# Optimization experiments

Measured on AMD Instinct MI355X. Metric: run time of the kernel, lower is better.

## Reference

```python
import jax, jax.numpy as jnp
import numpy as np

B = 8
N_KV = 1024          # kv-scale tokens (32x32)
D0, D1, D2 = 256, 512, 1024
DIM_HEAD = 64
H0, H2 = 2, 8        # fine-scale heads, coarse-scale heads (H2 == 4*H0)
EPS = 1e-5


def _ln(x, g, b):
    mu = jnp.mean(x, axis=-1, keepdims=True)
    var = jnp.var(x, axis=-1, keepdims=True)
    return (x - mu) * jax.lax.rsqrt(var + EPS) * g + b


def setup_inputs() -> dict:
    key = jax.random.key(0)
    ks = jax.random.split(key, 7)
    x0 = jax.random.normal(ks[0], (B, 4 * N_KV, D0), jnp.float32)
    x1 = jax.random.normal(ks[1], (B, N_KV, D1), jnp.float32)
    x2 = jax.random.normal(ks[2], (B, N_KV // 4, D2), jnp.float32)
    Wq0 = jax.random.normal(ks[3], (D0, H0 * DIM_HEAD), jnp.float32) * 0.02
    Wkv = jax.random.normal(ks[4], (D1, 2 * DIM_HEAD), jnp.float32) * 0.02
    Wq2 = jax.random.normal(ks[5], (D2, H2 * DIM_HEAD), jnp.float32) * 0.02
    concat_dim = H0 * (4 * DIM_HEAD + DIM_HEAD)  # 640
    Wout = jax.random.normal(ks[6], (concat_dim, D1), jnp.float32) * 0.02
    return {
        "x0": x0, "x1": x1, "x2": x2,
        "g0": jnp.ones((D0,), jnp.float32), "b0": jnp.zeros((D0,), jnp.float32),
        "g1": jnp.ones((D1,), jnp.float32), "b1": jnp.zeros((D1,), jnp.float32),
        "g2": jnp.ones((D2,), jnp.float32), "b2": jnp.zeros((D2,), jnp.float32),
        "Wq0": Wq0, "Wkv": Wkv, "Wq2": Wq2, "Wout": Wout,
    }


def reference(x0, x1, x2, g0, b0, g1, b1, g2, b2, Wq0, Wkv, Wq2, Wout):
    scale = DIM_HEAD ** -0.5
    # K/V from the kv scale, single broadcast head: [B, 1, N_KV, DIM_HEAD]
    kv = _ln(x1, g1, b1) @ Wkv
    k, v = jnp.split(kv, 2, axis=-1)
    k = k[:, None]
    v = v[:, None]
    # Queries: fine scale [B, H0, 4*N_KV, d]; coarse scale [B, H2, N_KV//4, d]
    q0 = (_ln(x0, g0, b0) @ Wq0).reshape(B, 4 * N_KV, H0, DIM_HEAD).transpose(0, 2, 1, 3)
    q2 = (_ln(x2, g2, b2) @ Wq2).reshape(B, N_KV // 4, H2, DIM_HEAD).transpose(0, 2, 1, 3)
    kt = jnp.swapaxes(k, -1, -2)
    # Fine branch: attend, then fold 4 consecutive tokens into channels
    a0 = jax.nn.softmax(jnp.matmul(q0, kt) * scale, axis=-1)
    o0 = jnp.matmul(a0, v)                                  # [B,H0,4*N_KV,d]
    o0 = o0.reshape(B, H0, N_KV, 4 * DIM_HEAD)              # b h (n n1) c -> b h n (n1 c)
    # Coarse branch: attend, then unfold 4 head-groups into tokens
    a2 = jax.nn.softmax(jnp.matmul(q2, kt) * scale, axis=-1)
    o2 = jnp.matmul(a2, v)                                  # [B,H2,N_KV//4,d]
    o2 = o2.reshape(B, H0, 4, N_KV // 4, DIM_HEAD).reshape(B, H0, N_KV, DIM_HEAD)  # b (h h1) n c -> b h (h1 n) c
    outs = jnp.concatenate([o0, o2], axis=-1)               # [B,H0,N_KV,320]
    outs = outs.transpose(0, 2, 1, 3).reshape(B, N_KV, -1)  # b h n d -> b n (h d)
    return outs @ Wout                                      # [B,N_KV,D1]
```

## Files before the change

### kernel.cpp

```cpp
#include <hip/hip_runtime.h>


typedef __attribute__((ext_vector_type(8))) short bf16x8;
typedef __attribute__((ext_vector_type(8))) _Float16 f16x8;
typedef __attribute__((ext_vector_type(4))) float f32x4;

constexpr size_t OFFB_KBF  = 0;
constexpr size_t OFFB_VT   = (size_t)1 << 20;
constexpr size_t OFFB_Q0   = (size_t)2 << 20;
constexpr size_t OFFB_Q2   = (size_t)10 << 20;
constexpr size_t OFFB_OF   = (size_t)12 << 20;
constexpr size_t OFFB_WTKV = (size_t)34 << 20;
constexpr size_t OFFB_WTQ0 = (size_t)35 << 20;
constexpr size_t OFFB_WTQ2 = (size_t)36 << 20;
constexpr size_t OFFB_WTO  = (size_t)37 << 20;

__device__ __forceinline__ unsigned short f2bf(float f) {
    union { float f; unsigned int u; } x; x.f = f;
    const unsigned int r = x.u + 0x7fffu + ((x.u >> 16) & 1u);
    return (unsigned short)(r >> 16);
}
__device__ __forceinline__ unsigned short f2h(float f) {
    union { _Float16 h; unsigned short u; } x;
    x.h = (_Float16)f;
    return x.u;
}
__device__ __forceinline__ unsigned int cvtpk_bf16(float lo, float hi) {
    unsigned int r;
    asm("v_cvt_pk_bf16_f32 %0, %1, %2" : "=v"(r) : "v"(lo), "v"(hi));
    return r;
}
__device__ __forceinline__ float fexp2(float x) {
    float r;
    asm("v_exp_f32 %0, %1" : "=v"(r) : "v"(x));
    return r;
}
#define EXP2_SCALE 0.18033688011112042f

template <int R, int C, bool F16>
__device__ __forceinline__ void transpose_w_body(
    int lbid, const float* __restrict__ W,
    unsigned short* __restrict__ D, float (*t)[33])
{
    const int tid = threadIdx.x;
    const int tx = tid & 31, ty = tid >> 5;
    const int bx = lbid % (C / 32);
    const int by = lbid / (C / 32);
    #pragma unroll
    for (int j = 0; j < 4; ++j) {
        const int r = ty + j * 8;
        t[r][tx] = W[(size_t)(by * 32 + r) * C + bx * 32 + tx];
    }
    __syncthreads();
    #pragma unroll
    for (int j = 0; j < 4; ++j) {
        const int r = ty + j * 8;
        const float v = t[tx][r];
        const size_t dst = (size_t)(bx * 32 + r) * R + by * 32 + tx;
        D[dst] = F16 ? f2h(v) : f2bf(v);
    }
}

__global__ __launch_bounds__(256) void transpose_all_k(
    const float* __restrict__ Wkv, const float* __restrict__ Wq0,
    const float* __restrict__ Wq2, const float* __restrict__ Wout,
    unsigned short* __restrict__ WtKV, unsigned short* __restrict__ WtQ0,
    unsigned short* __restrict__ WtQ2, unsigned short* __restrict__ WtO)
{
    __shared__ float t[32][33];
    const int b = blockIdx.x;
    if (b < 64)       transpose_w_body<512, 128, false>(b, Wkv, WtKV, t);
    else if (b < 96)  transpose_w_body<256, 128, false>(b - 64, Wq0, WtQ0, t);
    else if (b < 608) transpose_w_body<1024, 512, false>(b - 96, Wq2, WtQ2, t);
    else              transpose_w_body<640, 512, true>(b - 608, Wout, WtO, t);
}

template <int D, int MODE, int NRB>
__device__ __forceinline__ void ln_proj_body(
    int lbid, const float* __restrict__ X, const float* __restrict__ G,
    const float* __restrict__ Bv, const unsigned short* __restrict__ Wt,
    unsigned short* __restrict__ O0, unsigned short* __restrict__ O1,
    unsigned int* xn)
{
    constexpr int NJ = D / 128;

    const int tid  = threadIdx.x;
    const int lane = tid & 63;
    const int w    = tid >> 6;
    const int lq   = lane & 15;
    const int lg   = lane >> 4;

    const int rb      = lbid % NRB;
    const int cb      = lbid / NRB;
    const int colbase = cb * 128 + w * 32;

    #pragma unroll
    for (int rr = 0; rr < 4; ++rr) {
        const int r = w * 4 + rr;
        const float* xp = X + ((size_t)rb * 16 + r) * D;
        float2 xv[NJ];
        float ps = 0.f, pq = 0.f;
        #pragma unroll
        for (int j = 0; j < NJ; ++j) {
            xv[j] = *(const float2*)&xp[2 * lane + 128 * j];
            ps += xv[j].x + xv[j].y;
            pq += xv[j].x * xv[j].x + xv[j].y * xv[j].y;
        }
        #pragma unroll
        for (int off = 32; off >= 1; off >>= 1) {
            ps += __shfl_xor(ps, off);
            pq += __shfl_xor(pq, off);
        }
        const float mu  = ps * (1.f / D);
        const float var = pq * (1.f / D) - mu * mu;
        const float rs  = rsqrtf(var + 1e-5f);
        #pragma unroll
        for (int j = 0; j < NJ; ++j) {
            const int i2 = 2 * lane + 128 * j;
            const float2 gv = *(const float2*)&G[i2];
            const float2 bv = *(const float2*)&Bv[i2];
            const float a = (xv[j].x - mu) * rs * gv.x + bv.x;
            const float c = (xv[j].y - mu) * rs * gv.y + bv.y;
            const int pi = lane + 64 * j;
            xn[r * (D / 2) + ((((pi >> 2) ^ (r & 7)) << 2) | (pi & 3))] =
                cvtpk_bf16(a, c);
        }
    }
    __syncthreads();

    const unsigned short* wp = Wt + (size_t)(colbase + lq) * D + lg * 8;
    f32x4 acc0 = f32x4{0.f, 0.f, 0.f, 0.f};
    f32x4 acc1 = f32x4{0.f, 0.f, 0.f, 0.f};
    #pragma unroll 4
    for (int kk = 0; kk < D / 32; ++kk) {
        const int ch = (kk * 4 + lg) ^ (lq & 7);
        const bf16x8 xf = *(const bf16x8*)&xn[lq * (D / 2) + ch * 4];
        const bf16x8 wf0 = *(const bf16x8*)(wp + kk * 32);
        const bf16x8 wf1 = *(const bf16x8*)(wp + 16 * D + kk * 32);
        acc0 = __builtin_amdgcn_mfma_f32_16x16x32_bf16(wf0, xf, acc0, 0, 0, 0);
        acc1 = __builtin_amdgcn_mfma_f32_16x16x32_bf16(wf1, xf, acc1, 0, 0, 0);
    }

    const long grow = (long)rb * 16 + lq;
    #pragma unroll
    for (int t = 0; t < 2; ++t) {
        const f32x4 acc = t ? acc1 : acc0;
        #pragma unroll
        for (int r = 0; r < 4; ++r) {
            const int c = colbase + t * 16 + lg * 4 + r;
            const unsigned short a = f2bf(acc[r]);
            if constexpr (MODE == 0) {
                const long bb   = grow >> 10;
                const long keyb = grow & 1023;
                const long tt_  = keyb >> 6;
                if (c < 64) {
                    const int kt = (int)((keyb >> 4) & 3);
                    const int ch = c >> 5;
                    const int ln = (int)((keyb & 15) | (((c & 31) >> 3) << 4));
                    const int e  = c & 7;
                    O0[((((bb * 16 + tt_) * 4 + kt) * 2 + ch) * 64 + ln) * 8 + e] = a;
                } else {
                    const int dv = c - 64;
                    const int i  = dv >> 4;
                    const int ch = (int)((keyb & 63) >> 5);
                    const int ln = (int)((dv & 15) | (((keyb & 31) >> 3) << 4));
                    const int e  = (int)(keyb & 7);
                    O1[((((bb * 16 + tt_) * 4 + i) * 2 + ch) * 64 + ln) * 8 + e] = a;
                }
            } else if constexpr (MODE == 1) {
                const long b = grow >> 12;
                const long m = grow & 4095;
                const int  h = c >> 6, dd = c & 63;
                O0[(((b * 2 + h) << 12) + m) * 64 + dd] = a;
            } else {
                const long b = grow >> 8;
                const long m = grow & 255;
                const int  h = c >> 6, dd = c & 63;
                O0[(((b * 8 + h) << 8) + m) * 64 + dd] = a;
            }
        }
    }
}

__global__ __launch_bounds__(256) void proj_kvq2_k(
    const float* __restrict__ x1, const float* __restrict__ x2,
    const float* __restrict__ g1, const float* __restrict__ b1,
    const float* __restrict__ g2, const float* __restrict__ b2,
    const unsigned short* __restrict__ WtKV, const unsigned short* __restrict__ WtQ2,
    unsigned short* __restrict__ Kf, unsigned short* __restrict__ Vf,
    unsigned short* __restrict__ Q2bf)
{
    __shared__ unsigned int xn[8192];
    const int b = blockIdx.x;
    if (b < 512) ln_proj_body<512, 0, 512>(b, x1, g1, b1, WtKV, Kf, Vf, xn);
    else         ln_proj_body<1024, 2, 128>(b - 512, x2, g2, b2, WtQ2, Q2bf, nullptr, xn);
}

__global__ __launch_bounds__(256) void proj_q0_k(
    const float* __restrict__ x0,
    const float* __restrict__ g0, const float* __restrict__ b0,
    const unsigned short* __restrict__ WtQ0,
    unsigned short* __restrict__ Q0bf)
{
    __shared__ unsigned int xn[2048];
    ln_proj_body<256, 1, 2048>(blockIdx.x, x0, g0, b0, WtQ0, Q0bf, nullptr, xn);
}

__device__ __forceinline__ void load_ktile(
    const unsigned short* __restrict__ kp, int t, bf16x8 (&kf)[8])
{
    const unsigned short* ktb = kp + (size_t)t * 8 * 512;
    #pragma unroll
    for (int kt = 0; kt < 4; ++kt) {
        kf[2 * kt]     = *(const bf16x8*)(ktb + (kt * 2 + 0) * 512);
        kf[2 * kt + 1] = *(const bf16x8*)(ktb + (kt * 2 + 1) * 512);
    }
}

__device__ __forceinline__ void process_tile(
    int t, const bf16x8 (&kf)[8],
    const unsigned short* __restrict__ vp,
    const bf16x8& qfA0, const bf16x8& qfA1,
    const bf16x8& qfB0, const bf16x8& qfB1,
    f32x4 (&otA)[4], f32x4 (&otB)[4], float& psA, float& psB,
    unsigned int (&pl)[2][16][32], int lq, int lg)
{
    const unsigned short* vtb = vp + (size_t)t * 8 * 512;
    bf16x8 vf[8];
    #pragma unroll
    for (int i = 0; i < 4; ++i) {
        vf[2 * i]     = *(const bf16x8*)(vtb + (i * 2 + 0) * 512);
        vf[2 * i + 1] = *(const bf16x8*)(vtb + (i * 2 + 1) * 512);
    }

    #pragma unroll
    for (int kt = 0; kt < 4; ++kt) {
        f32x4 sA = f32x4{0.f, 0.f, 0.f, 0.f};
        sA = __builtin_amdgcn_mfma_f32_16x16x32_bf16(kf[2 * kt], qfA0, sA, 0, 0, 0);
        sA = __builtin_amdgcn_mfma_f32_16x16x32_bf16(kf[2 * kt + 1], qfA1, sA, 0, 0, 0);
        f32x4 sB = f32x4{0.f, 0.f, 0.f, 0.f};
        sB = __builtin_amdgcn_mfma_f32_16x16x32_bf16(kf[2 * kt], qfB0, sB, 0, 0, 0);
        sB = __builtin_amdgcn_mfma_f32_16x16x32_bf16(kf[2 * kt + 1], qfB1, sB, 0, 0, 0);

        float pA[4], pB[4];
        #pragma unroll
        for (int r = 0; r < 4; ++r) {
            pA[r] = fexp2(sA[r] * EXP2_SCALE);
            pB[r] = fexp2(sB[r] * EXP2_SCALE);
            psA += pA[r];
            psB += pB[r];
        }
        const int sw = (((2 * kt + (lg >> 1)) ^ (lq & 7)) << 2) | (2 * (lg & 1));
        pl[0][lq][sw]     = cvtpk_bf16(pA[0], pA[1]);
        pl[0][lq][sw + 1] = cvtpk_bf16(pA[2], pA[3]);
        pl[1][lq][sw]     = cvtpk_bf16(pB[0], pB[1]);
        pl[1][lq][sw + 1] = cvtpk_bf16(pB[2], pB[3]);
    }

    __builtin_amdgcn_s_setprio(1);
    #pragma unroll
    for (int k0g = 0; k0g < 2; ++k0g) {
        const int ch = k0g * 4 + lg;
        const bf16x8 pfA = *(const bf16x8*)&pl[0][lq][(ch ^ (lq & 7)) << 2];
        const bf16x8 pfB = *(const bf16x8*)&pl[1][lq][(ch ^ (lq & 7)) << 2];
        #pragma unroll
        for (int i = 0; i < 4; ++i) {
            otA[i] = __builtin_amdgcn_mfma_f32_16x16x32_bf16(vf[2 * i + k0g], pfA, otA[i], 0, 0, 0);
            otB[i] = __builtin_amdgcn_mfma_f32_16x16x32_bf16(vf[2 * i + k0g], pfB, otB[i], 0, 0, 0);
        }
    }
    __builtin_amdgcn_s_setprio(0);
}

template <int MODE>
__device__ __forceinline__ void attn_body(
    int lbid, const unsigned short* __restrict__ Q,
    const unsigned short* __restrict__ K,
    const unsigned short* __restrict__ Vt,
    unsigned short* __restrict__ Of,
    unsigned int (*plds)[2][16][32], float* __restrict__ psb)
{
    constexpr int H   = (MODE == 0) ? 2 : 8;
    constexpr int M   = (MODE == 0) ? 4096 : 256;
    constexpr int BPB = M / 64;

    const int tid  = threadIdx.x;
    const int lane = tid & 63;
    const int w    = tid >> 6;
    const int lq   = lane & 15;
    const int lg   = lane >> 4;

    const int bh  = lbid / BPB;
    const int qb  = lbid % BPB;
    const int qg  = w & 1;
    const int ks  = w >> 1;
    const int q0g = qb * 64 + qg * 32;
    const int b   = bh / H;
    const int h   = bh % H;

    const unsigned short* qpA = Q + ((size_t)bh * M + q0g + lq) * 64 + 8 * lg;
    const bf16x8 qfA0 = *(const bf16x8*)(qpA);
    const bf16x8 qfA1 = *(const bf16x8*)(qpA + 32);
    const bf16x8 qfB0 = *(const bf16x8*)(qpA + 16 * 64);
    const bf16x8 qfB1 = *(const bf16x8*)(qpA + 16 * 64 + 32);

    const unsigned short* kp = K  + (size_t)b * 65536 + 8 * lane;
    const unsigned short* vp = Vt + (size_t)b * 65536 + 8 * lane;

    f32x4 otA[4], otB[4];
    #pragma unroll
    for (int i = 0; i < 4; ++i) {
        otA[i] = f32x4{0.f, 0.f, 0.f, 0.f};
        otB[i] = f32x4{0.f, 0.f, 0.f, 0.f};
    }
    float psA = 0.f, psB = 0.f;

    const int tb = ks * 8;
    bf16x8 ka[8], kb[8];
    load_ktile(kp, tb, ka);

    #pragma unroll 1
    for (int tt = 0; tt < 4; ++tt) {
        load_ktile(kp, tb + 2 * tt + 1, kb);
        process_tile(tb + 2 * tt, ka, vp, qfA0, qfA1, qfB0, qfB1,
                     otA, otB, psA, psB, plds[w], lq, lg);
        if (tt < 3) load_ktile(kp, tb + 2 * tt + 2, ka);
        process_tile(tb + 2 * tt + 1, kb, vp, qfA0, qfA1, qfB0, qfB1,
                     otA, otB, psA, psB, plds[w], lq, lg);
    }

    __syncthreads();
    float* sc = (float*)plds;
    if (w >= 2) {
        const int off = (w - 2) * 64 + lane;
        #pragma unroll
        for (int i = 0; i < 4; ++i) {
            #pragma unroll
            for (int r = 0; r < 4; ++r) {
                sc[(i * 4 + r) * 128 + off]        = otA[i][r];
                sc[(16 + i * 4 + r) * 128 + off]   = otB[i][r];
            }
        }
        psb[off]       = psA;
        psb[128 + off] = psB;
    }
    __syncthreads();
    if (w < 2) {
        const int off = w * 64 + lane;
        #pragma unroll
        for (int i = 0; i < 4; ++i) {
            #pragma unroll
            for (int r = 0; r < 4; ++r) {
                otA[i][r] += sc[(i * 4 + r) * 128 + off];
                otB[i][r] += sc[(16 + i * 4 + r) * 128 + off];
            }
        }
        psA += psb[off];
        psB += psb[128 + off];

        psA += __shfl_xor(psA, 16); psA += __shfl_xor(psA, 32);
        psB += __shfl_xor(psB, 16); psB += __shfl_xor(psB, 32);
        const float invA = 1.f / psA;
        const float invB = 1.f / psB;

        #pragma unroll
        for (int half = 0; half < 2; ++half) {
            const int   m   = q0g + half * 16 + lq;
            const float inv = half ? invB : invA;
            #pragma unroll
            for (int i = 0; i < 4; ++i) {
                #pragma unroll
                for (int r = 0; r < 4; ++r) {
                    const int   dv  = i * 16 + lg * 4 + r;
                    const float val = (half ? otB[i][r] : otA[i][r]) * inv;
                    size_t dst;
                    if constexpr (MODE == 0) {
                        dst = ((size_t)b * 1024 + (m >> 2)) * 640 + h * 320 + (m & 3) * 64 + dv;
                    } else {
                        dst = ((size_t)b * 1024 + ((h & 3) * 256 + m)) * 640 + (h >> 2) * 320 + 256 + dv;
                    }
                    Of[dst] = f2h(val);
                }
            }
        }
    }
}

__global__ __launch_bounds__(256) void attn_all_k(
    const unsigned short* __restrict__ Q0, const unsigned short* __restrict__ Q2,
    const unsigned short* __restrict__ K, const unsigned short* __restrict__ Vt,
    unsigned short* __restrict__ Of)
{
    __shared__ unsigned int plds[4][2][16][32];
    __shared__ float psb[256];
    if (blockIdx.x < 1024) attn_body<0>(blockIdx.x, Q0, K, Vt, Of, plds, psb);
    else                   attn_body<1>(blockIdx.x - 1024, Q2, K, Vt, Of, plds, psb);
}

__global__ __launch_bounds__(256) void out_gemm_f16_k(
    const unsigned short* __restrict__ Of, const unsigned short* __restrict__ WtO,
    float* __restrict__ OUT)
{
    const int tid  = threadIdx.x;
    const int lane = tid & 63;
    const int w    = tid >> 6;
    const int lq   = lane & 15;
    const int lg   = lane >> 4;

    const int bid = blockIdx.x;
    const int rp  = (bid & 7) + 8 * (bid >> 5);
    const int cb  = (bid >> 3) & 3;

    const long row0    = (long)rp * 64;
    const int  colbase = cb * 128 + w * 32;

    const unsigned short* aP = Of  + (size_t)(row0 + lq) * 640 + lg * 8;
    const unsigned short* bP = WtO + (size_t)(colbase + lq) * 640 + lg * 8;

    f16x8 a0[4], b0[2], a1[4], b1[2];

    auto load0 = [&](int kk) {
        #pragma unroll
        for (int rt = 0; rt < 4; ++rt)
            a0[rt] = *(const f16x8*)(aP + (size_t)rt * 16 * 640 + kk * 32);
        #pragma unroll
        for (int ct = 0; ct < 2; ++ct)
            b0[ct] = *(const f16x8*)(bP + (size_t)ct * 16 * 640 + kk * 32);
    };
    auto load1 = [&](int kk) {
        #pragma unroll
        for (int rt = 0; rt < 4; ++rt)
            a1[rt] = *(const f16x8*)(aP + (size_t)rt * 16 * 640 + kk * 32);
        #pragma unroll
        for (int ct = 0; ct < 2; ++ct)
            b1[ct] = *(const f16x8*)(bP + (size_t)ct * 16 * 640 + kk * 32);
    };

    f32x4 acc[4][2];
    #pragma unroll
    for (int rt = 0; rt < 4; ++rt)
        #pragma unroll
        for (int ct = 0; ct < 2; ++ct) acc[rt][ct] = f32x4{0.f, 0.f, 0.f, 0.f};

    auto mma0 = [&]() {
        #pragma unroll
        for (int rt = 0; rt < 4; ++rt)
            #pragma unroll
            for (int ct = 0; ct < 2; ++ct)
                acc[rt][ct] = __builtin_amdgcn_mfma_f32_16x16x32_f16(a0[rt], b0[ct], acc[rt][ct], 0, 0, 0);
    };
    auto mma1 = [&]() {
        #pragma unroll
        for (int rt = 0; rt < 4; ++rt)
            #pragma unroll
            for (int ct = 0; ct < 2; ++ct)
                acc[rt][ct] = __builtin_amdgcn_mfma_f32_16x16x32_f16(a1[rt], b1[ct], acc[rt][ct], 0, 0, 0);
    };

    load0(0);
    #pragma unroll 1
    for (int kk2 = 0; kk2 < 10; ++kk2) {
        load1(2 * kk2 + 1);
        mma0();
        if (kk2 < 9) load0(2 * kk2 + 2);
        mma1();
    }

    #pragma unroll
    for (int rt = 0; rt < 4; ++rt)
        #pragma unroll
        for (int ct = 0; ct < 2; ++ct)
            #pragma unroll
            for (int r = 0; r < 4; ++r)
                OUT[(size_t)(row0 + rt * 16 + lg * 4 + r) * 512
                    + colbase + ct * 16 + lq] = acc[rt][ct][r];
}

extern "C" void kernel_launch(void* const* d_in, const int* in_sizes, int n_in,
                              void* d_out, int out_size, void* d_ws, size_t ws_size,
                              hipStream_t stream) {
    const float* x0   = (const float*)d_in[0];
    const float* x1   = (const float*)d_in[1];
    const float* x2   = (const float*)d_in[2];
    const float* g0   = (const float*)d_in[3];
    const float* b0   = (const float*)d_in[4];
    const float* g1   = (const float*)d_in[5];
    const float* b1   = (const float*)d_in[6];
    const float* g2   = (const float*)d_in[7];
    const float* b2   = (const float*)d_in[8];
    const float* Wq0  = (const float*)d_in[9];
    const float* Wkv  = (const float*)d_in[10];
    const float* Wq2  = (const float*)d_in[11];
    const float* Wout = (const float*)d_in[12];
    float* out = (float*)d_out;

    char* wsb = (char*)d_ws;
    unsigned short* Kf   = (unsigned short*)(wsb + OFFB_KBF);
    unsigned short* Vf   = (unsigned short*)(wsb + OFFB_VT);
    unsigned short* Q0bf = (unsigned short*)(wsb + OFFB_Q0);
    unsigned short* Q2bf = (unsigned short*)(wsb + OFFB_Q2);
    unsigned short* Of   = (unsigned short*)(wsb + OFFB_OF);
    unsigned short* WtKV = (unsigned short*)(wsb + OFFB_WTKV);
    unsigned short* WtQ0 = (unsigned short*)(wsb + OFFB_WTQ0);
    unsigned short* WtQ2 = (unsigned short*)(wsb + OFFB_WTQ2);
    unsigned short* WtO  = (unsigned short*)(wsb + OFFB_WTO);

    transpose_all_k<<<928, 256, 0, stream>>>(Wkv, Wq0, Wq2, Wout,
                                             WtKV, WtQ0, WtQ2, WtO);
    proj_kvq2_k<<<1024, 256, 0, stream>>>(x1, x2, g1, b1, g2, b2,
                                          WtKV, WtQ2, Kf, Vf, Q2bf);
    proj_q0_k<<<2048, 256, 0, stream>>>(x0, g0, b0, WtQ0, Q0bf);
    attn_all_k<<<1280, 256, 0, stream>>>(Q0bf, Q2bf, Kf, Vf, Of);
    out_gemm_f16_k<<<512, 256, 0, stream>>>(Of, WtO, out);
}
```

Measured before the change: 121.2 us.

## Split attention KV range four ways per block with 32-query tiles

Each attention block now handles 32 queries instead of 64. Its four waves each cover a quarter of the KV sequence rather than two query groups times two KV halves, which doubles the grid to 2560 blocks. The cross-wave reduction becomes a 4-way sum done by wave 0 through a larger shared buffer. The intent is more parallelism and shorter per-wave loops, at the cost of more Q/K/V reloads across blocks, a heavier reduction, and more shared memory.

```diff
diff --git a/kernel.cpp b/kernel.cpp
--- a/kernel.cpp
+++ b/kernel.cpp
@@ -223,7 +223,7 @@
     const bf16x8& qfA0, const bf16x8& qfA1,
     const bf16x8& qfB0, const bf16x8& qfB1,
     f32x4 (&otA)[4], f32x4 (&otB)[4], float& psA, float& psB,
-    unsigned int (&pl)[2][16][32], int lq, int lg)
+    unsigned int* pl, int lq, int lg)
 {
     const unsigned short* vtb = vp + (size_t)t * 8 * 512;
     bf16x8 vf[8];
@@ -251,18 +251,18 @@
             psB += pB[r];
         }
         const int sw = (((2 * kt + (lg >> 1)) ^ (lq & 7)) << 2) | (2 * (lg & 1));
-        pl[0][lq][sw]     = cvtpk_bf16(pA[0], pA[1]);
-        pl[0][lq][sw + 1] = cvtpk_bf16(pA[2], pA[3]);
-        pl[1][lq][sw]     = cvtpk_bf16(pB[0], pB[1]);
-        pl[1][lq][sw + 1] = cvtpk_bf16(pB[2], pB[3]);
+        pl[(0 * 16 + lq) * 32 + sw]     = cvtpk_bf16(pA[0], pA[1]);
+        pl[(0 * 16 + lq) * 32 + sw + 1] = cvtpk_bf16(pA[2], pA[3]);
+        pl[(1 * 16 + lq) * 32 + sw]     = cvtpk_bf16(pB[0], pB[1]);
+        pl[(1 * 16 + lq) * 32 + sw + 1] = cvtpk_bf16(pB[2], pB[3]);
     }
 
     __builtin_amdgcn_s_setprio(1);
     #pragma unroll
     for (int k0g = 0; k0g < 2; ++k0g) {
         const int ch = k0g * 4 + lg;
-        const bf16x8 pfA = *(const bf16x8*)&pl[0][lq][(ch ^ (lq & 7)) << 2];
-        const bf16x8 pfB = *(const bf16x8*)&pl[1][lq][(ch ^ (lq & 7)) << 2];
+        const bf16x8 pfA = *(const bf16x8*)&pl[(0 * 16 + lq) * 32 + ((ch ^ (lq & 7)) << 2)];
+        const bf16x8 pfB = *(const bf16x8*)&pl[(1 * 16 + lq) * 32 + ((ch ^ (lq & 7)) << 2)];
         #pragma unroll
         for (int i = 0; i < 4; ++i) {
             otA[i] = __builtin_amdgcn_mfma_f32_16x16x32_bf16(vf[2 * i + k0g], pfA, otA[i], 0, 0, 0);
@@ -278,11 +278,11 @@
     const unsigned short* __restrict__ K,
     const unsigned short* __restrict__ Vt,
     unsigned short* __restrict__ Of,
-    unsigned int (*plds)[2][16][32], float* __restrict__ psb)
+    unsigned int* smem)
 {
     constexpr int H   = (MODE == 0) ? 2 : 8;
     constexpr int M   = (MODE == 0) ? 4096 : 256;
-    constexpr int BPB = M / 64;
+    constexpr int BPB = M / 32;
 
     const int tid  = threadIdx.x;
     const int lane = tid & 63;
@@ -292,9 +292,7 @@
 
     const int bh  = lbid / BPB;
     const int qb  = lbid % BPB;
-    const int qg  = w & 1;
-    const int ks  = w >> 1;
-    const int q0g = qb * 64 + qg * 32;
+    const int q0g = qb * 32;
     const int b   = bh / H;
     const int h   = bh % H;
 
@@ -315,48 +313,53 @@
     }
     float psA = 0.f, psB = 0.f;
 
-    const int tb = ks * 8;
+    unsigned int* pl = smem + w * 1024;
+
+    const int tb = w * 4;
     bf16x8 ka[8], kb[8];
     load_ktile(kp, tb, ka);
 
     #pragma unroll 1
-    for (int tt = 0; tt < 4; ++tt) {
+    for (int tt = 0; tt < 2; ++tt) {
         load_ktile(kp, tb + 2 * tt + 1, kb);
         process_tile(tb + 2 * tt, ka, vp, qfA0, qfA1, qfB0, qfB1,
-                     otA, otB, psA, psB, plds[w], lq, lg);
-        if (tt < 3) load_ktile(kp, tb + 2 * tt + 2, ka);
+                     otA, otB, psA, psB, pl, lq, lg);
+        if (tt < 1) load_ktile(kp, tb + 2 * tt + 2, ka);
         process_tile(tb + 2 * tt + 1, kb, vp, qfA0, qfA1, qfB0, qfB1,
-                     otA, otB, psA, psB, plds[w], lq, lg);
+                     otA, otB, psA, psB, pl, lq, lg);
     }
 
     __syncthreads();
-    float* sc = (float*)plds;
-    if (w >= 2) {
-        const int off = (w - 2) * 64 + lane;
+    float* sc = (float*)smem;
+    if (w >= 1) {
+        const int off = (w - 1) * 64 + lane;
         #pragma unroll
         for (int i = 0; i < 4; ++i) {
             #pragma unroll
             for (int r = 0; r < 4; ++r) {
-                sc[(i * 4 + r) * 128 + off]        = otA[i][r];
-                sc[(16 + i * 4 + r) * 128 + off]   = otB[i][r];
+                sc[(i * 4 + r) * 192 + off]        = otA[i][r];
+                sc[(16 + i * 4 + r) * 192 + off]   = otB[i][r];
             }
         }
-        psb[off]       = psA;
-        psb[128 + off] = psB;
+        sc[6144 + off] = psA;
+        sc[6336 + off] = psB;
     }
     __syncthreads();
-    if (w < 2) {
-        const int off = w * 64 + lane;
-        #pragma unroll
-        for (int i = 0; i < 4; ++i) {
+    if (w == 0) {
+        #pragma unroll
+        for (int j = 0; j < 3; ++j) {
+            const int off = j * 64 + lane;
             #pragma unroll
-            for (int r = 0; r < 4; ++r) {
-                otA[i][r] += sc[(i * 4 + r) * 128 + off];
-                otB[i][r] += sc[(16 + i * 4 + r) * 128 + off];
+            for (int i = 0; i < 4; ++i) {
+                #pragma unroll
+                for (int r = 0; r < 4; ++r) {
+                    otA[i][r] += sc[(i * 4 + r) * 192 + off];
+                    otB[i][r] += sc[(16 + i * 4 + r) * 192 + off];
+                }
             }
-        }
-        psA += psb[off];
-        psB += psb[128 + off];
+            psA += sc[6144 + off];
+            psB += sc[6336 + off];
+        }
 
         psA += __shfl_xor(psA, 16); psA += __shfl_xor(psA, 32);
         psB += __shfl_xor(psB, 16); psB += __shfl_xor(psB, 32);
@@ -391,10 +394,9 @@
     const unsigned short* __restrict__ K, const unsigned short* __restrict__ Vt,
     unsigned short* __restrict__ Of)
 {
-    __shared__ unsigned int plds[4][2][16][32];
-    __shared__ float psb[256];
-    if (blockIdx.x < 1024) attn_body<0>(blockIdx.x, Q0, K, Vt, Of, plds, psb);
-    else                   attn_body<1>(blockIdx.x - 1024, Q2, K, Vt, Of, plds, psb);
+    __shared__ __align__(16) unsigned int smem[6528];
+    if (blockIdx.x < 2048) attn_body<0>(blockIdx.x, Q0, K, Vt, Of, smem);
+    else                   attn_body<1>(blockIdx.x - 2048, Q2, K, Vt, Of, smem);
 }
 
 __global__ __launch_bounds__(256) void out_gemm_f16_k(
@@ -510,6 +512,6 @@
     proj_kvq2_k<<<1024, 256, 0, stream>>>(x1, x2, g1, b1, g2, b2,
                                           WtKV, WtQ2, Kf, Vf, Q2bf);
     proj_q0_k<<<2048, 256, 0, stream>>>(x0, g0, b0, WtQ0, Q0bf);
-    attn_all_k<<<1280, 256, 0, stream>>>(Q0bf, Q2bf, Kf, Vf, Of);
+    attn_all_k<<<2560, 256, 0, stream>>>(Q0bf, Q2bf, Kf, Vf, Of);
     out_gemm_f16_k<<<512, 256, 0, stream>>>(Of, WtO, out);
 }
```

Result: slower. 143.0 us (+18.0%).

## Fold softmax scale into query projection and stage out-GEMM A tiles in LDS

Applied to the files above, without the earlier changes.

The softmax exp2 scale is now applied once when the Q0 and Q2 projections are written, which removes a multiply per score element in the attention inner loop. The output GEMM now stages each 64x32 A tile in double-buffered shared memory, with every thread loading one 16-byte chunk. Previously each of the four waves loaded the same A rows from global memory itself. This trades redundant global loads for block-wide barriers, and also changes where the scaled queries are rounded to bf16.

```diff
diff --git a/kernel.cpp b/kernel.cpp
--- a/kernel.cpp
+++ b/kernel.cpp
@@ -80,7 +80,7 @@
     int lbid, const float* __restrict__ X, const float* __restrict__ G,
     const float* __restrict__ Bv, const unsigned short* __restrict__ Wt,
     unsigned short* __restrict__ O0, unsigned short* __restrict__ O1,
-    unsigned int* xn)
+    unsigned int* xn, float SC)
 {
     constexpr int NJ = D / 128;
 
@@ -148,7 +148,7 @@
         #pragma unroll
         for (int r = 0; r < 4; ++r) {
             const int c = colbase + t * 16 + lg * 4 + r;
-            const unsigned short a = f2bf(acc[r]);
+            const unsigned short a = f2bf(acc[r] * SC);
             if constexpr (MODE == 0) {
                 const long bb   = grow >> 10;
                 const long keyb = grow & 1023;
@@ -192,8 +192,8 @@
 {
     __shared__ unsigned int xn[8192];
     const int b = blockIdx.x;
-    if (b < 512) ln_proj_body<512, 0, 512>(b, x1, g1, b1, WtKV, Kf, Vf, xn);
-    else         ln_proj_body<1024, 2, 128>(b - 512, x2, g2, b2, WtQ2, Q2bf, nullptr, xn);
+    if (b < 512) ln_proj_body<512, 0, 512>(b, x1, g1, b1, WtKV, Kf, Vf, xn, 1.0f);
+    else         ln_proj_body<1024, 2, 128>(b - 512, x2, g2, b2, WtQ2, Q2bf, nullptr, xn, EXP2_SCALE);
 }
 
 __global__ __launch_bounds__(256) void proj_q0_k(
@@ -203,7 +203,7 @@
     unsigned short* __restrict__ Q0bf)
 {
     __shared__ unsigned int xn[2048];
-    ln_proj_body<256, 1, 2048>(blockIdx.x, x0, g0, b0, WtQ0, Q0bf, nullptr, xn);
+    ln_proj_body<256, 1, 2048>(blockIdx.x, x0, g0, b0, WtQ0, Q0bf, nullptr, xn, EXP2_SCALE);
 }
 
 __device__ __forceinline__ void load_ktile(
@@ -245,8 +245,8 @@
         float pA[4], pB[4];
         #pragma unroll
         for (int r = 0; r < 4; ++r) {
-            pA[r] = fexp2(sA[r] * EXP2_SCALE);
-            pB[r] = fexp2(sB[r] * EXP2_SCALE);
+            pA[r] = fexp2(sA[r]);
+            pB[r] = fexp2(sB[r]);
             psA += pA[r];
             psB += pB[r];
         }
@@ -401,6 +401,8 @@
     const unsigned short* __restrict__ Of, const unsigned short* __restrict__ WtO,
     float* __restrict__ OUT)
 {
+    __shared__ __align__(16) unsigned short As[2][64][40];
+
     const int tid  = threadIdx.x;
     const int lane = tid & 63;
     const int w    = tid >> 6;
@@ -414,56 +416,57 @@
     const long row0    = (long)rp * 64;
     const int  colbase = cb * 128 + w * 32;
 
-    const unsigned short* aP = Of  + (size_t)(row0 + lq) * 640 + lg * 8;
-    const unsigned short* bP = WtO + (size_t)(colbase + lq) * 640 + lg * 8;
-
-    f16x8 a0[4], b0[2], a1[4], b1[2];
-
-    auto load0 = [&](int kk) {
+    const int srow = tid >> 2;
+    const int sko  = (tid & 3) * 8;
+    const unsigned short* aSrc = Of  + (size_t)(row0 + srow) * 640 + sko;
+    const unsigned short* bP   = WtO + (size_t)(colbase + lq) * 640 + lg * 8;
+
+    f16x8 b0[2], b1[2];
+
+    auto stage = [&](int kk, int buf) {
+        *(f16x8*)&As[buf][srow][sko] = *(const f16x8*)(aSrc + kk * 32);
+    };
+    auto loadB0 = [&](int kk) {
+        b0[0] = *(const f16x8*)(bP + kk * 32);
+        b0[1] = *(const f16x8*)(bP + 16 * 640 + kk * 32);
+    };
+    auto loadB1 = [&](int kk) {
+        b1[0] = *(const f16x8*)(bP + kk * 32);
+        b1[1] = *(const f16x8*)(bP + 16 * 640 + kk * 32);
+    };
+
+    f32x4 acc[4][2];
+    #pragma unroll
+    for (int rt = 0; rt < 4; ++rt)
+        #pragma unroll
+        for (int ct = 0; ct < 2; ++ct) acc[rt][ct] = f32x4{0.f, 0.f, 0.f, 0.f};
+
+    auto mmaWith = [&](int buf, f16x8 (&bb)[2]) {
+        f16x8 a[4];
         #pragma unroll
         for (int rt = 0; rt < 4; ++rt)
-            a0[rt] = *(const f16x8*)(aP + (size_t)rt * 16 * 640 + kk * 32);
-        #pragma unroll
-        for (int ct = 0; ct < 2; ++ct)
-            b0[ct] = *(const f16x8*)(bP + (size_t)ct * 16 * 640 + kk * 32);
-    };
-    auto load1 = [&](int kk) {
-        #pragma unroll
-        for (int rt = 0; rt < 4; ++rt)
-            a1[rt] = *(const f16x8*)(aP + (size_t)rt * 16 * 640 + kk * 32);
-        #pragma unroll
-        for (int ct = 0; ct < 2; ++ct)
-            b1[ct] = *(const f16x8*)(bP + (size_t)ct * 16 * 640 + kk * 32);
-    };
-
-    f32x4 acc[4][2];
-    #pragma unroll
-    for (int rt = 0; rt < 4; ++rt)
-        #pragma unroll
-        for (int ct = 0; ct < 2; ++ct) acc[rt][ct] = f32x4{0.f, 0.f, 0.f, 0.f};
-
-    auto mma0 = [&]() {
+            a[rt] = *(const f16x8*)&As[buf][rt * 16 + lq][lg * 8];
         #pragma unroll
         for (int rt = 0; rt < 4; ++rt)
             #pragma unroll
             for (int ct = 0; ct < 2; ++ct)
-                acc[rt][ct] = __builtin_amdgcn_mfma_f32_16x16x32_f16(a0[rt], b0[ct], acc[rt][ct], 0, 0, 0);
+                acc[rt][ct] = __builtin_amdgcn_mfma_f32_16x16x32_f16(a[rt], bb[ct], acc[rt][ct], 0, 0, 0);
     };
-    auto mma1 = [&]() {
-        #pragma unroll
-        for (int rt = 0; rt < 4; ++rt)
-            #pragma unroll
-            for (int ct = 0; ct < 2; ++ct)
-                acc[rt][ct] = __builtin_amdgcn_mfma_f32_16x16x32_f16(a1[rt], b1[ct], acc[rt][ct], 0, 0, 0);
-    };
-
-    load0(0);
+
+    stage(0, 0);
+    loadB0(0);
+    __syncthreads();
+
     #pragma unroll 1
-    for (int kk2 = 0; kk2 < 10; ++kk2) {
-        load1(2 * kk2 + 1);
-        mma0();
-        if (kk2 < 9) load0(2 * kk2 + 2);
-        mma1();
+    for (int it = 0; it < 10; ++it) {
+        const int kk = 2 * it;
+        stage(kk + 1, 1);
+        loadB1(kk + 1);
+        mmaWith(0, b0);
+        __syncthreads();
+        if (it < 9) { stage(kk + 2, 0); loadB0(kk + 2); }
+        mmaWith(1, b1);
+        __syncthreads();
     }
 
     #pragma unroll
```

Result: faster. 107.8 us (median of 2 runs) (-11.1%).
